# Kernel tuning notes

Hardware: AMD Instinct MI355X
Metric: run time of the kernel (lower is better)

The kernel has to match this reference:

```python
import jax, jax.numpy as jnp
import numpy as np

B, T, K, H = 256, 2048, 64, 256
NUM_PRED = 512


def setup_inputs() -> dict:
    key = jax.random.key(0)
    ks = jax.random.split(key, 13)
    s = 0.05
    G = 4 * H
    return {
        "input": jax.random.normal(ks[0], (B, T), jnp.float32),
        "conv_w": jax.random.normal(ks[1], (K,), jnp.float32) * s,
        "conv_b": jax.random.normal(ks[2], (K,), jnp.float32) * s,
        "W_ih0": jax.random.normal(ks[3], (G, K), jnp.float32) * s,
        "W_hh0": jax.random.normal(ks[4], (G, H), jnp.float32) * s,
        "b_ih0": jax.random.normal(ks[5], (G,), jnp.float32) * s,
        "b_hh0": jax.random.normal(ks[6], (G,), jnp.float32) * s,
        "W_ih1": jax.random.normal(ks[7], (G, H), jnp.float32) * s,
        "W_hh1": jax.random.normal(ks[8], (G, H), jnp.float32) * s,
        "b_ih1": jax.random.normal(ks[9], (G,), jnp.float32) * s,
        "b_hh1": jax.random.normal(ks[10], (G,), jnp.float32) * s,
        "lin_w": jax.random.normal(ks[11], (1, H), jnp.float32) * s,
        "lin_b": jax.random.normal(ks[12], (1,), jnp.float32) * s,
        "num_predictions": NUM_PRED,
    }


def _cell(x, h, c, Wi, Wh, bi, bh):
    # PyTorch LSTM cell: gate order i, f, g, o
    g = x @ Wi.T + h @ Wh.T + bi + bh
    i, f, gg, o = jnp.split(g, 4, axis=-1)
    i = jax.nn.sigmoid(i)
    f = jax.nn.sigmoid(f)
    gg = jnp.tanh(gg)
    o = jax.nn.sigmoid(o)
    c_new = f * c + i * gg
    h_new = o * jnp.tanh(c_new)
    return h_new, c_new


def reference(input, conv_w, conv_b, W_ih0, W_hh0, b_ih0, b_hh0,
              W_ih1, W_hh1, b_ih1, b_hh1, lin_w, lin_b, num_predictions):
    Bn, Tn = input.shape
    Kn = conv_w.shape[0]
    Hh = W_hh0.shape[1]

    # cnn: [B,1,T] -> Conv1d(1,K,1) -> [B,K,T] -> ReLU -> torch.reshape to (B,T,K)
    # NOTE: original uses reshape (not transpose); replicate faithfully.
    c_raw = jax.nn.relu(input[:, None, :] * conv_w[None, :, None] + conv_b[None, :, None])  # [B,K,T]
    c_out = c_raw.reshape(Bn, Tn, Kn)  # faithful reshape-as-in-source

    def step(carry, x):
        h0, c0, h1, c1 = carry
        h0, c0 = _cell(x, h0, c0, W_ih0, W_hh0, b_ih0, b_hh0)
        h1, c1 = _cell(h0, h1, c1, W_ih1, W_hh1, b_ih1, b_hh1)
        return (h0, c0, h1, c1), None

    z = jnp.zeros((Bn, Hh), input.dtype)
    carry, _ = jax.lax.scan(step, (z, z, z, z), jnp.swapaxes(c_out, 0, 1))  # scan over T
    pred0 = carry[2] @ lin_w.T + lin_b  # [B,1], output of last warmup step

    def ar_step(carry, _):
        h0, c0, h1, c1, last = carry
        x = jax.nn.relu(last[:, None] * conv_w[None, :] + conv_b[None, :])  # [B,K]
        h0, c0 = _cell(x, h0, c0, W_ih0, W_hh0, b_ih0, b_hh0)
        h1, c1 = _cell(h0, h1, c1, W_ih1, W_hh1, b_ih1, b_hh1)
        p = (h1 @ lin_w.T + lin_b)[:, 0]  # [B]
        return (h0, c0, h1, c1, p), p

    init = (*carry, pred0[:, 0])
    _, preds = jax.lax.scan(ar_step, init, None, length=num_predictions - 1)  # [P-1, B]
    return jnp.concatenate([pred0, preds.T], axis=1)  # [B, num_predictions]
```

## Files before the change

### kernel.cpp

```cpp
#include <hip/hip_runtime.h>
#include <hip/hip_bf16.h>
#include <cstdint>

#define TT 2048
#define NPRED 512
#define NSTEP (TT + NPRED)

typedef _Float16 f16;
typedef __attribute__((ext_vector_type(8))) _Float16 f16x8;
typedef __attribute__((ext_vector_type(4))) float f32x4;

#define WB0_OFF   0u
#define WB1_OFF   655360u
#define BIAS0_OFF 1703936u
#define BIAS1_OFF 1708032u
#define HX0_OFF   1712128u
#define HX1_OFF   1974272u
#define FLAG_OFF  2236416u
#define PACC_OFF  2244608u

static __device__ __forceinline__ float sigmoidf_(float x) {
    return 1.0f / (1.0f + __expf(-x));
}

static __device__ __forceinline__ uint2 ld8u(const unsigned short* p) {
    unsigned long long v = __hip_atomic_load((const unsigned long long*)p,
                                             __ATOMIC_RELAXED, __HIP_MEMORY_SCOPE_AGENT);
    uint2 r; r.x = (unsigned)v; r.y = (unsigned)(v >> 32); return r;
}
static __device__ __forceinline__ float ld1a(const float* p) {
    unsigned v = __hip_atomic_load((const unsigned*)p,
                                   __ATOMIC_RELAXED, __HIP_MEMORY_SCOPE_AGENT);
    return __uint_as_float(v);
}
static __device__ __forceinline__ void st1a(float* p, float v) {
    __hip_atomic_store((unsigned*)p, __float_as_uint(v),
                       __ATOMIC_RELAXED, __HIP_MEMORY_SCOPE_AGENT);
}
static __device__ __forceinline__ void st4a(unsigned* p, unsigned v) {
    __hip_atomic_store(p, v, __ATOMIC_RELAXED, __HIP_MEMORY_SCOPE_AGENT);
}
static __device__ __forceinline__ unsigned short f16bits(float x) {
    union { f16 h; unsigned short u; } cv;
    cv.h = (f16)x;
    return cv.u;
}

#define N0_ELEM 327680
#define N1_ELEM 524288

__global__ __launch_bounds__(256) void prep_kernel(
    const float* __restrict__ W_ih0, const float* __restrict__ W_hh0,
    const float* __restrict__ b_ih0, const float* __restrict__ b_hh0,
    const float* __restrict__ W_ih1, const float* __restrict__ W_hh1,
    const float* __restrict__ b_ih1, const float* __restrict__ b_hh1,
    f16* __restrict__ WB0, f16* __restrict__ WB1,
    float* __restrict__ bias0P, float* __restrict__ bias1P,
    unsigned int* __restrict__ flags, float* __restrict__ p_part)
{
    int idx = blockIdx.x * 256 + threadIdx.x;
    if (idx < N0_ELEM) {
        int e = idx & 7, l = (idx >> 3) & 63;
        int rest = idx >> 9;
        int fr = rest % 10, sw = rest / 10;
        int w = sw & 3, slice = sw >> 2;
        int q = l & 3, jj = (l & 15) >> 2;
        int row = q * 256 + slice * 16 + 4 * w + jj;
        int k = fr * 32 + (l >> 4) * 8 + e;
        float v = (k < 64) ? W_ih0[row * 64 + k] : W_hh0[row * 256 + (k - 64)];
        WB0[idx] = (f16)v;
    } else if (idx < N0_ELEM + N1_ELEM) {
        int i2 = idx - N0_ELEM;
        int e = i2 & 7, l = (i2 >> 3) & 63;
        int rest = i2 >> 9;
        int fr = rest & 15, sw = rest >> 4;
        int w = sw & 3, slice = sw >> 2;
        int q = l & 3, jj = (l & 15) >> 2;
        int row = q * 256 + slice * 16 + 4 * w + jj;
        int k = fr * 32 + (l >> 4) * 8 + e;
        float v = (k < 256) ? W_ih1[row * 256 + k] : W_hh1[row * 256 + (k - 256)];
        WB1[i2] = (f16)v;
    } else if (idx < N0_ELEM + N1_ELEM + 1024) {
        int r = idx - (N0_ELEM + N1_ELEM);
        int j = r >> 2, q = r & 3;
        bias0P[r] = b_ih0[q * 256 + j] + b_hh0[q * 256 + j];
    } else if (idx < N0_ELEM + N1_ELEM + 2048) {
        int r = idx - (N0_ELEM + N1_ELEM + 1024);
        int j = r >> 2, q = r & 3;
        bias1P[r] = b_ih1[q * 256 + j] + b_hh1[q * 256 + j];
    } else if (idx < N0_ELEM + N1_ELEM + 2048 + 2048) {
        flags[idx - (N0_ELEM + N1_ELEM + 2048)] = 0u;
    } else if (idx < N0_ELEM + N1_ELEM + 2048 + 2048 + 8192) {
        p_part[idx - (N0_ELEM + N1_ELEM + 2048 + 2048)] = 0.f;
    }
}

__global__ __launch_bounds__(256) void fused_kernel(
    const float* __restrict__ input,
    const float* __restrict__ conv_w, const float* __restrict__ conv_b,
    const f16* __restrict__ WB0, const f16* __restrict__ WB1,
    const float* __restrict__ bias0P, const float* __restrict__ bias1P,
    const float* __restrict__ lin_w, const float* __restrict__ lin_b,
    unsigned short* hx0, unsigned short* hx1,
    unsigned int* flags, float* p_part,
    float* __restrict__ out)
{
    const int t = threadIdx.x;
    const int lane = t & 63, w = t >> 6;
    const int g = blockIdx.x & 15, slice = blockIdx.x >> 4;

    __shared__ __align__(16) f16 Ah[18 * 65 * 8];
    __shared__ __align__(16) float gbuf0[16 * 68 + 4];
    __shared__ __align__(16) float gbuf1[16 * 68 + 4];
    __shared__ float cw_s[64], cb_s[64], lw_s[256];
    __shared__ float p_lds[16];

    f16x8 B0[10], B1[16];
    {
        const f16* p0 = WB0 + ((size_t)(slice * 4 + w) * 10 * 64 + lane) * 8;
        #pragma unroll
        for (int f = 0; f < 10; ++f) B0[f] = *(const f16x8*)(p0 + f * 512);
        const f16* p1 = WB1 + ((size_t)(slice * 4 + w) * 16 * 64 + lane) * 8;
        #pragma unroll
        for (int f = 0; f < 16; ++f) B1[f] = *(const f16x8*)(p1 + f * 512);
    }

    if (t < 64) { cw_s[t] = conv_w[t]; cb_s[t] = conv_b[t]; }
    lw_s[t] = lin_w[t];

    #pragma unroll
    for (int i = 0; i < 4; ++i) {
        int c = t + 256 * i;
        int d = ((2 + (c >> 6)) * 65 + (c & 63)) * 8;
        f16x8 z = {};
        *(f16x8*)(Ah + d) = z;
    }

    const int ub = t >> 4, uj = t & 15;
    const int jg = slice * 16 + uj;
    const float4 bs0 = *(const float4*)(bias0P + 4 * jg);
    const float4 bs1 = *(const float4*)(bias1P + 4 * jg);
    float c0 = 0.f, c1 = 0.f;
    const float linb = lin_b[0];

    const int rb = t & 15;
    const int rest = t >> 4;
    const int bg0 = g * 16;

    unsigned int* fl0 = flags + (size_t)g * 64;
    unsigned int* cnp = flags + (size_t)(16 + g) * 64;

    __syncthreads();

    #pragma unroll 1
    for (int k = 0; k < TT; ++k) {
        if (k >= 1) {
            const unsigned short* s0 = hx0 + (size_t)((k - 1) & 1) * 65536 + (size_t)(bg0 + rb) * 256;
            #pragma unroll
            for (int it = 0; it < 2; ++it) {
                int oct = rest + 16 * it;
                uint2 a = ld8u(s0 + oct * 8);
                uint2 b = ld8u(s0 + oct * 8 + 4);
                int d = ((2 + (oct >> 2)) * 65 + (rb + 16 * (oct & 3))) * 8;
                *(uint4*)(Ah + d) = make_uint4(a.x, a.y, b.x, b.y);
            }
        }
        if (k >= 2) {
            const unsigned short* s1 = hx1 + (size_t)((k - 1) & 1) * 65536 + (size_t)(bg0 + rb) * 256;
            #pragma unroll
            for (int it = 0; it < 2; ++it) {
                int oct = rest + 16 * it;
                uint2 a = ld8u(s1 + oct * 8);
                uint2 b = ld8u(s1 + oct * 8 + 4);
                int d = ((10 + (oct >> 2)) * 65 + (rb + 16 * (oct & 3))) * 8;
                *(uint4*)(Ah + d) = make_uint4(a.x, a.y, b.x, b.y);
            }
        }
        if (t < 128) {
            int rb2 = t & 15, xoct = t >> 4;
            int k0 = xoct * 8;
            const float* inprow = input + (size_t)(bg0 + rb2) * TT + ((k & 31) << 6);
            float cwv = cw_s[k >> 5], cbv = cb_s[k >> 5];
            f16x8 hv;
            #pragma unroll
            for (int e = 0; e < 8; ++e)
                hv[e] = (f16)fmaxf(inprow[k0 + e] * cwv + cbv, 0.f);
            int d = ((xoct >> 2) * 65 + (rb2 + 16 * (xoct & 3))) * 8;
            *(f16x8*)(Ah + d) = hv;
        }
        __syncthreads();

        {
            f32x4 acc = {0.f, 0.f, 0.f, 0.f};
            #pragma unroll
            for (int f = 0; f < 10; ++f) {
                f16x8 a = *(const f16x8*)(Ah + (f * 65 + lane) * 8);
                acc = __builtin_amdgcn_mfma_f32_16x16x32_f16(a, B0[f], acc, 0, 0, 0);
            }
            int rr = w * 16 + (lane & 15);
            int bb = (lane >> 4) * 4;
            #pragma unroll
            for (int qq = 0; qq < 4; ++qq) gbuf0[(bb + qq) * 68 + rr] = acc[qq];
        }
        if (k >= 1) {
            f32x4 acc = {0.f, 0.f, 0.f, 0.f};
            #pragma unroll
            for (int f = 0; f < 16; ++f) {
                f16x8 a = *(const f16x8*)(Ah + ((2 + f) * 65 + lane) * 8);
                acc = __builtin_amdgcn_mfma_f32_16x16x32_f16(a, B1[f], acc, 0, 0, 0);
            }
            int rr = w * 16 + (lane & 15);
            int bb = (lane >> 4) * 4;
            #pragma unroll
            for (int qq = 0; qq < 4; ++qq) gbuf1[(bb + qq) * 68 + rr] = acc[qq];
        }
        __syncthreads();

        {
            float4 gv = *(const float4*)(gbuf0 + ub * 68 + uj * 4);
            float gi = gv.x + bs0.x, gf = gv.y + bs0.y, gg = gv.z + bs0.z, go = gv.w + bs0.w;
            float cn = sigmoidf_(gf) * c0 + sigmoidf_(gi) * tanhf(gg);
            float hn = sigmoidf_(go) * tanhf(cn);
            c0 = cn;
            unsigned short hb = f16bits(hn);
            int oth = __shfl_xor((int)hb, 1);
            if (!(uj & 1)) {
                unsigned word = (unsigned)hb | ((unsigned)(oth & 0xffff) << 16);
                st4a((unsigned*)(hx0 + (size_t)(k & 1) * 65536 + (size_t)(bg0 + ub) * 256 + jg), word);
            }
        }
        if (k >= 1) {
            float4 gv = *(const float4*)(gbuf1 + ub * 68 + uj * 4);
            float gi = gv.x + bs1.x, gf = gv.y + bs1.y, gg = gv.z + bs1.z, go = gv.w + bs1.w;
            float cn = sigmoidf_(gf) * c1 + sigmoidf_(gi) * tanhf(gg);
            float hn = sigmoidf_(go) * tanhf(cn);
            c1 = cn;
            unsigned short hb = f16bits(hn);
            int oth = __shfl_xor((int)hb, 1);
            if (!(uj & 1)) {
                unsigned word = (unsigned)hb | ((unsigned)(oth & 0xffff) << 16);
                st4a((unsigned*)(hx1 + (size_t)(k & 1) * 65536 + (size_t)(bg0 + ub) * 256 + jg), word);
            }
        }
        __syncthreads();
        if (t == 0) {
            __hip_atomic_fetch_add(fl0, 1u, __ATOMIC_RELAXED, __HIP_MEMORY_SCOPE_AGENT);
            unsigned tgt = 16u * (unsigned)(k + 1);
            while (__hip_atomic_load(fl0, __ATOMIC_RELAXED, __HIP_MEMORY_SCOPE_AGENT) < tgt)
                __builtin_amdgcn_s_sleep(1);
        }
        __syncthreads();
    }

    #pragma unroll 1
    for (int k = TT; k < NSTEP; ++k) {
        {
            const unsigned short* s0 = hx0 + (size_t)((k - 1) & 1) * 65536 + (size_t)(bg0 + rb) * 256;
            const unsigned short* s1 = hx1 + (size_t)((k - 1) & 1) * 65536 + (size_t)(bg0 + rb) * 256;
            #pragma unroll
            for (int it = 0; it < 2; ++it) {
                int oct = rest + 16 * it;
                uint2 a0 = ld8u(s0 + oct * 8);
                uint2 b0 = ld8u(s0 + oct * 8 + 4);
                int d = ((2 + (oct >> 2)) * 65 + (rb + 16 * (oct & 3))) * 8;
                *(uint4*)(Ah + d) = make_uint4(a0.x, a0.y, b0.x, b0.y);
                uint2 a1 = ld8u(s1 + oct * 8);
                uint2 b1 = ld8u(s1 + oct * 8 + 4);
                d = ((10 + (oct >> 2)) * 65 + (rb + 16 * (oct & 3))) * 8;
                *(uint4*)(Ah + d) = make_uint4(a1.x, a1.y, b1.x, b1.y);
            }
        }
        __syncthreads();

        {
            f32x4 acc = {0.f, 0.f, 0.f, 0.f};
            #pragma unroll
            for (int f = 0; f < 16; ++f) {
                f16x8 a = *(const f16x8*)(Ah + ((2 + f) * 65 + lane) * 8);
                acc = __builtin_amdgcn_mfma_f32_16x16x32_f16(a, B1[f], acc, 0, 0, 0);
            }
            int rr = w * 16 + (lane & 15);
            int bb = (lane >> 4) * 4;
            #pragma unroll
            for (int qq = 0; qq < 4; ++qq) gbuf1[(bb + qq) * 68 + rr] = acc[qq];
        }
        __syncthreads();

        {
            float4 gv = *(const float4*)(gbuf1 + ub * 68 + uj * 4);
            float gi = gv.x + bs1.x, gf = gv.y + bs1.y, gg = gv.z + bs1.z, go = gv.w + bs1.w;
            float cn = sigmoidf_(gf) * c1 + sigmoidf_(gi) * tanhf(gg);
            float hn = sigmoidf_(go) * tanhf(cn);
            c1 = cn;
            unsigned short hb = f16bits(hn);
            int oth = __shfl_xor((int)hb, 1);
            if (!(uj & 1)) {
                unsigned word = (unsigned)hb | ((unsigned)(oth & 0xffff) << 16);
                st4a((unsigned*)(hx1 + (size_t)(k & 1) * 65536 + (size_t)(bg0 + ub) * 256 + jg), word);
            }
            float pp = hn * lw_s[jg];
            pp += __shfl_xor(pp, 1);
            pp += __shfl_xor(pp, 2);
            pp += __shfl_xor(pp, 4);
            pp += __shfl_xor(pp, 8);
            if (uj == 0)
                st1a(p_part + (size_t)(k & 1) * 4096 + (size_t)slice * 256 + (bg0 + ub), pp);
        }
        __syncthreads();
        if (t == 0) {
            __hip_atomic_fetch_add(cnp, 1u, __ATOMIC_RELAXED, __HIP_MEMORY_SCOPE_AGENT);
            unsigned tgt = 16u * (unsigned)(k - TT + 1);
            while (__hip_atomic_load(cnp, __ATOMIC_RELAXED, __HIP_MEMORY_SCOPE_AGENT) < tgt)
                __builtin_amdgcn_s_sleep(1);
        }
        __syncthreads();

        if (t < 16) {
            const float* pb = p_part + (size_t)(k & 1) * 4096;
            float ps = 0.f;
            #pragma unroll
            for (int sl = 0; sl < 16; ++sl) ps += ld1a(pb + sl * 256 + bg0 + t);
            float p = ps + linb;
            p_lds[t] = p;
            if (slice == 0) out[(size_t)(bg0 + t) * NPRED + (k - TT)] = p;
        }
        if (k == NSTEP - 1) break;
        __syncthreads();

        if (t < 128) {
            int rb2 = t & 15, xoct = t >> 4;
            int k0 = xoct * 8;
            float p = p_lds[rb2];
            f16x8 hv;
            #pragma unroll
            for (int e = 0; e < 8; ++e)
                hv[e] = (f16)fmaxf(p * cw_s[k0 + e] + cb_s[k0 + e], 0.f);
            int d = ((xoct >> 2) * 65 + (rb2 + 16 * (xoct & 3))) * 8;
            *(f16x8*)(Ah + d) = hv;
        }
        __syncthreads();

        {
            f32x4 acc = {0.f, 0.f, 0.f, 0.f};
            #pragma unroll
            for (int f = 0; f < 10; ++f) {
                f16x8 a = *(const f16x8*)(Ah + (f * 65 + lane) * 8);
                acc = __builtin_amdgcn_mfma_f32_16x16x32_f16(a, B0[f], acc, 0, 0, 0);
            }
            int rr = w * 16 + (lane & 15);
            int bb = (lane >> 4) * 4;
            #pragma unroll
            for (int qq = 0; qq < 4; ++qq) gbuf0[(bb + qq) * 68 + rr] = acc[qq];
        }
        __syncthreads();
        {
            float4 gv = *(const float4*)(gbuf0 + ub * 68 + uj * 4);
            float gi = gv.x + bs0.x, gf = gv.y + bs0.y, gg = gv.z + bs0.z, go = gv.w + bs0.w;
            float cn = sigmoidf_(gf) * c0 + sigmoidf_(gi) * tanhf(gg);
            float hn = sigmoidf_(go) * tanhf(cn);
            c0 = cn;
            unsigned short hb = f16bits(hn);
            int oth = __shfl_xor((int)hb, 1);
            if (!(uj & 1)) {
                unsigned word = (unsigned)hb | ((unsigned)(oth & 0xffff) << 16);
                st4a((unsigned*)(hx0 + (size_t)(k & 1) * 65536 + (size_t)(bg0 + ub) * 256 + jg), word);
            }
        }
        __syncthreads();
        if (t == 0) {
            __hip_atomic_fetch_add(fl0, 1u, __ATOMIC_RELAXED, __HIP_MEMORY_SCOPE_AGENT);
            unsigned tgt = 16u * (unsigned)(k + 1);
            while (__hip_atomic_load(fl0, __ATOMIC_RELAXED, __HIP_MEMORY_SCOPE_AGENT) < tgt)
                __builtin_amdgcn_s_sleep(1);
        }
        __syncthreads();
    }
}

extern "C" void kernel_launch(void* const* d_in, const int* in_sizes, int n_in,
                              void* d_out, int out_size, void* d_ws, size_t ws_size,
                              hipStream_t stream) {
    const float* input  = (const float*)d_in[0];
    const float* conv_w = (const float*)d_in[1];
    const float* conv_b = (const float*)d_in[2];
    const float* W_ih0  = (const float*)d_in[3];
    const float* W_hh0  = (const float*)d_in[4];
    const float* b_ih0  = (const float*)d_in[5];
    const float* b_hh0  = (const float*)d_in[6];
    const float* W_ih1  = (const float*)d_in[7];
    const float* W_hh1  = (const float*)d_in[8];
    const float* b_ih1  = (const float*)d_in[9];
    const float* b_hh1  = (const float*)d_in[10];
    const float* lin_w  = (const float*)d_in[11];
    const float* lin_b  = (const float*)d_in[12];
    float* out = (float*)d_out;

    uint8_t* ws = (uint8_t*)d_ws;
    f16* WB0 = (f16*)(ws + WB0_OFF);
    f16* WB1 = (f16*)(ws + WB1_OFF);
    float* bias0P = (float*)(ws + BIAS0_OFF);
    float* bias1P = (float*)(ws + BIAS1_OFF);
    unsigned short* hx0 = (unsigned short*)(ws + HX0_OFF);
    unsigned short* hx1 = (unsigned short*)(ws + HX1_OFF);
    unsigned int* flags = (unsigned int*)(ws + FLAG_OFF);
    float* p_part = (float*)(ws + PACC_OFF);

    prep_kernel<<<3376, 256, 0, stream>>>(W_ih0, W_hh0, b_ih0, b_hh0,
                                          W_ih1, W_hh1, b_ih1, b_hh1,
                                          WB0, WB1, bias0P, bias1P, flags, p_part);

    fused_kernel<<<256, 256, 0, stream>>>(input, conv_w, conv_b,
                                          WB0, WB1, bias0P, bias1P,
                                          lin_w, lin_b, hx0, hx1, flags, p_part, out);
}
```

Baseline: 9.296 ms.

## Transpose hidden-state exchange layout to feature-pair-major and compute two units per thread

The global hidden-state exchange buffers change from batch-major f16 to feature-pair-major 32-bit words. Each of 128 threads now computes two hidden units and writes a packed word directly, with no shuffle to pair halves. Each reader thread issues 4 coalesced 8-byte atomic loads per layer and scatters them into the MFMA LDS layout, instead of 4 scattered loads per row. The prediction partial sum now reduces across waves through a small LDS buffer, which adds one extra barrier per autoregressive step.

```diff
diff --git a/kernel.cpp b/kernel.cpp
--- a/kernel.cpp
+++ b/kernel.cpp
@@ -9,6 +9,7 @@
 typedef _Float16 f16;
 typedef __attribute__((ext_vector_type(8))) _Float16 f16x8;
 typedef __attribute__((ext_vector_type(4))) float f32x4;
+typedef unsigned long long u64;
 
 #define WB0_OFF   0u
 #define WB1_OFF   655360u
@@ -23,10 +24,8 @@
     return 1.0f / (1.0f + __expf(-x));
 }
 
-static __device__ __forceinline__ uint2 ld8u(const unsigned short* p) {
-    unsigned long long v = __hip_atomic_load((const unsigned long long*)p,
-                                             __ATOMIC_RELAXED, __HIP_MEMORY_SCOPE_AGENT);
-    uint2 r; r.x = (unsigned)v; r.y = (unsigned)(v >> 32); return r;
+static __device__ __forceinline__ u64 lda8w(const u64* p) {
+    return __hip_atomic_load(p, __ATOMIC_RELAXED, __HIP_MEMORY_SCOPE_AGENT);
 }
 static __device__ __forceinline__ float ld1a(const float* p) {
     unsigned v = __hip_atomic_load((const unsigned*)p,
@@ -101,7 +100,7 @@
     const f16* __restrict__ WB0, const f16* __restrict__ WB1,
     const float* __restrict__ bias0P, const float* __restrict__ bias1P,
     const float* __restrict__ lin_w, const float* __restrict__ lin_b,
-    unsigned short* hx0, unsigned short* hx1,
+    unsigned* hx0w, unsigned* hx1w,
     unsigned int* flags, float* p_part,
     float* __restrict__ out)
 {
@@ -112,8 +111,9 @@
     __shared__ __align__(16) f16 Ah[18 * 65 * 8];
     __shared__ __align__(16) float gbuf0[16 * 68 + 4];
     __shared__ __align__(16) float gbuf1[16 * 68 + 4];
-    __shared__ float cw_s[64], cb_s[64], lw_s[256];
+    __shared__ float cw_s[64], cb_s[64];
     __shared__ float p_lds[16];
+    __shared__ float p_part4[2][16];
 
     f16x8 B0[10], B1[16];
     {
@@ -126,7 +126,6 @@
     }
 
     if (t < 64) { cw_s[t] = conv_w[t]; cb_s[t] = conv_b[t]; }
-    lw_s[t] = lin_w[t];
 
     #pragma unroll
     for (int i = 0; i < 4; ++i) {
@@ -136,15 +135,21 @@
         *(f16x8*)(Ah + d) = z;
     }
 
-    const int ub = t >> 4, uj = t & 15;
-    const int jg = slice * 16 + uj;
-    const float4 bs0 = *(const float4*)(bias0P + 4 * jg);
-    const float4 bs1 = *(const float4*)(bias1P + 4 * jg);
-    float c0 = 0.f, c1 = 0.f;
+    const int jploc = t >> 4;
+    const int ucol  = t & 15;
+    const int jga   = slice * 16 + jploc * 2;
+    float4 ba0 = make_float4(0.f,0.f,0.f,0.f), bb0 = ba0, ba1 = ba0, bb1 = ba0;
+    float lwa = 0.f, lwb = 0.f;
+    if (t < 128) {
+        ba0 = *(const float4*)(bias0P + 4 * jga);
+        bb0 = *(const float4*)(bias0P + 4 * jga + 4);
+        ba1 = *(const float4*)(bias1P + 4 * jga);
+        bb1 = *(const float4*)(bias1P + 4 * jga + 4);
+        lwa = lin_w[jga];
+        lwb = lin_w[jga + 1];
+    }
+    float c0a = 0.f, c0b = 0.f, c1a = 0.f, c1b = 0.f;
     const float linb = lin_b[0];
-
-    const int rb = t & 15;
-    const int rest = t >> 4;
     const int bg0 = g * 16;
 
     unsigned int* fl0 = flags + (size_t)g * 64;
@@ -155,25 +160,31 @@
     #pragma unroll 1
     for (int k = 0; k < TT; ++k) {
         if (k >= 1) {
-            const unsigned short* s0 = hx0 + (size_t)((k - 1) & 1) * 65536 + (size_t)(bg0 + rb) * 256;
-            #pragma unroll
-            for (int it = 0; it < 2; ++it) {
-                int oct = rest + 16 * it;
-                uint2 a = ld8u(s0 + oct * 8);
-                uint2 b = ld8u(s0 + oct * 8 + 4);
-                int d = ((2 + (oct >> 2)) * 65 + (rb + 16 * (oct & 3))) * 8;
-                *(uint4*)(Ah + d) = make_uint4(a.x, a.y, b.x, b.y);
+            const unsigned* s0 = hx0w + (size_t)((k - 1) & 1) * 32768;
+            #pragma unroll
+            for (int p = 0; p < 4; ++p) {
+                int row = p * 32 + (t >> 3);
+                int cp  = t & 7;
+                u64 v = lda8w((const u64*)(s0 + row * 256 + bg0 + 2 * cp));
+                int f  = 2 + (row >> 4);
+                int la = 2 * cp + 16 * ((row & 15) >> 2);
+                int byte = (f * 65 + la) * 16 + 4 * (row & 3);
+                *(unsigned*)((char*)Ah + byte)      = (unsigned)v;
+                *(unsigned*)((char*)Ah + byte + 16) = (unsigned)(v >> 32);
             }
         }
         if (k >= 2) {
-            const unsigned short* s1 = hx1 + (size_t)((k - 1) & 1) * 65536 + (size_t)(bg0 + rb) * 256;
-            #pragma unroll
-            for (int it = 0; it < 2; ++it) {
-                int oct = rest + 16 * it;
-                uint2 a = ld8u(s1 + oct * 8);
-                uint2 b = ld8u(s1 + oct * 8 + 4);
-                int d = ((10 + (oct >> 2)) * 65 + (rb + 16 * (oct & 3))) * 8;
-                *(uint4*)(Ah + d) = make_uint4(a.x, a.y, b.x, b.y);
+            const unsigned* s1 = hx1w + (size_t)((k - 1) & 1) * 32768;
+            #pragma unroll
+            for (int p = 0; p < 4; ++p) {
+                int row = p * 32 + (t >> 3);
+                int cp  = t & 7;
+                u64 v = lda8w((const u64*)(s1 + row * 256 + bg0 + 2 * cp));
+                int f  = 10 + (row >> 4);
+                int la = 2 * cp + 16 * ((row & 15) >> 2);
+                int byte = (f * 65 + la) * 16 + 4 * (row & 3);
+                *(unsigned*)((char*)Ah + byte)      = (unsigned)v;
+                *(unsigned*)((char*)Ah + byte + 16) = (unsigned)(v >> 32);
             }
         }
         if (t < 128) {
@@ -216,30 +227,30 @@
         }
         __syncthreads();
 
-        {
-            float4 gv = *(const float4*)(gbuf0 + ub * 68 + uj * 4);
-            float gi = gv.x + bs0.x, gf = gv.y + bs0.y, gg = gv.z + bs0.z, go = gv.w + bs0.w;
-            float cn = sigmoidf_(gf) * c0 + sigmoidf_(gi) * tanhf(gg);
-            float hn = sigmoidf_(go) * tanhf(cn);
-            c0 = cn;
-            unsigned short hb = f16bits(hn);
-            int oth = __shfl_xor((int)hb, 1);
-            if (!(uj & 1)) {
-                unsigned word = (unsigned)hb | ((unsigned)(oth & 0xffff) << 16);
-                st4a((unsigned*)(hx0 + (size_t)(k & 1) * 65536 + (size_t)(bg0 + ub) * 256 + jg), word);
-            }
-        }
-        if (k >= 1) {
-            float4 gv = *(const float4*)(gbuf1 + ub * 68 + uj * 4);
-            float gi = gv.x + bs1.x, gf = gv.y + bs1.y, gg = gv.z + bs1.z, go = gv.w + bs1.w;
-            float cn = sigmoidf_(gf) * c1 + sigmoidf_(gi) * tanhf(gg);
-            float hn = sigmoidf_(go) * tanhf(cn);
-            c1 = cn;
-            unsigned short hb = f16bits(hn);
-            int oth = __shfl_xor((int)hb, 1);
-            if (!(uj & 1)) {
-                unsigned word = (unsigned)hb | ((unsigned)(oth & 0xffff) << 16);
-                st4a((unsigned*)(hx1 + (size_t)(k & 1) * 65536 + (size_t)(bg0 + ub) * 256 + jg), word);
+        if (t < 128) {
+            const float* gp = gbuf0 + ucol * 68 + jploc * 8;
+            float4 g0 = *(const float4*)(gp);
+            float4 g1 = *(const float4*)(gp + 4);
+            float cna = sigmoidf_(g0.y + ba0.y) * c0a + sigmoidf_(g0.x + ba0.x) * tanhf(g0.z + ba0.z);
+            float hna = sigmoidf_(g0.w + ba0.w) * tanhf(cna);
+            c0a = cna;
+            float cnb = sigmoidf_(g1.y + bb0.y) * c0b + sigmoidf_(g1.x + bb0.x) * tanhf(g1.z + bb0.z);
+            float hnb = sigmoidf_(g1.w + bb0.w) * tanhf(cnb);
+            c0b = cnb;
+            unsigned word = (unsigned)f16bits(hna) | ((unsigned)f16bits(hnb) << 16);
+            st4a(hx0w + (size_t)(k & 1) * 32768 + (size_t)(slice * 8 + jploc) * 256 + (bg0 + ucol), word);
+            if (k >= 1) {
+                const float* hp = gbuf1 + ucol * 68 + jploc * 8;
+                float4 h0v = *(const float4*)(hp);
+                float4 h1v = *(const float4*)(hp + 4);
+                float cka = sigmoidf_(h0v.y + ba1.y) * c1a + sigmoidf_(h0v.x + ba1.x) * tanhf(h0v.z + ba1.z);
+                float hka = sigmoidf_(h0v.w + ba1.w) * tanhf(cka);
+                c1a = cka;
+                float ckb = sigmoidf_(h1v.y + bb1.y) * c1b + sigmoidf_(h1v.x + bb1.x) * tanhf(h1v.z + bb1.z);
+                float hkb = sigmoidf_(h1v.w + bb1.w) * tanhf(ckb);
+                c1b = ckb;
+                unsigned wrd = (unsigned)f16bits(hka) | ((unsigned)f16bits(hkb) << 16);
+                st4a(hx1w + (size_t)(k & 1) * 32768 + (size_t)(slice * 8 + jploc) * 256 + (bg0 + ucol), wrd);
             }
         }
         __syncthreads();
@@ -255,19 +266,21 @@
     #pragma unroll 1
     for (int k = TT; k < NSTEP; ++k) {
         {
-            const unsigned short* s0 = hx0 + (size_t)((k - 1) & 1) * 65536 + (size_t)(bg0 + rb) * 256;
-            const unsigned short* s1 = hx1 + (size_t)((k - 1) & 1) * 65536 + (size_t)(bg0 + rb) * 256;
-            #pragma unroll
-            for (int it = 0; it < 2; ++it) {
-                int oct = rest + 16 * it;
-                uint2 a0 = ld8u(s0 + oct * 8);
-                uint2 b0 = ld8u(s0 + oct * 8 + 4);
-                int d = ((2 + (oct >> 2)) * 65 + (rb + 16 * (oct & 3))) * 8;
-                *(uint4*)(Ah + d) = make_uint4(a0.x, a0.y, b0.x, b0.y);
-                uint2 a1 = ld8u(s1 + oct * 8);
-                uint2 b1 = ld8u(s1 + oct * 8 + 4);
-                d = ((10 + (oct >> 2)) * 65 + (rb + 16 * (oct & 3))) * 8;
-                *(uint4*)(Ah + d) = make_uint4(a1.x, a1.y, b1.x, b1.y);
+            const unsigned* s0 = hx0w + (size_t)((k - 1) & 1) * 32768;
+            const unsigned* s1 = hx1w + (size_t)((k - 1) & 1) * 32768;
+            #pragma unroll
+            for (int p = 0; p < 4; ++p) {
+                int row = p * 32 + (t >> 3);
+                int cp  = t & 7;
+                u64 v0 = lda8w((const u64*)(s0 + row * 256 + bg0 + 2 * cp));
+                int la = 2 * cp + 16 * ((row & 15) >> 2);
+                int byte0 = ((2 + (row >> 4)) * 65 + la) * 16 + 4 * (row & 3);
+                *(unsigned*)((char*)Ah + byte0)      = (unsigned)v0;
+                *(unsigned*)((char*)Ah + byte0 + 16) = (unsigned)(v0 >> 32);
+                u64 v1 = lda8w((const u64*)(s1 + row * 256 + bg0 + 2 * cp));
+                int byte1 = ((10 + (row >> 4)) * 65 + la) * 16 + 4 * (row & 3);
+                *(unsigned*)((char*)Ah + byte1)      = (unsigned)v1;
+                *(unsigned*)((char*)Ah + byte1 + 16) = (unsigned)(v1 >> 32);
             }
         }
         __syncthreads();
@@ -286,25 +299,27 @@
         }
         __syncthreads();
 
-        {
-            float4 gv = *(const float4*)(gbuf1 + ub * 68 + uj * 4);
-            float gi = gv.x + bs1.x, gf = gv.y + bs1.y, gg = gv.z + bs1.z, go = gv.w + bs1.w;
-            float cn = sigmoidf_(gf) * c1 + sigmoidf_(gi) * tanhf(gg);
-            float hn = sigmoidf_(go) * tanhf(cn);
-            c1 = cn;
-            unsigned short hb = f16bits(hn);
-            int oth = __shfl_xor((int)hb, 1);
-            if (!(uj & 1)) {
-                unsigned word = (unsigned)hb | ((unsigned)(oth & 0xffff) << 16);
-                st4a((unsigned*)(hx1 + (size_t)(k & 1) * 65536 + (size_t)(bg0 + ub) * 256 + jg), word);
-            }
-            float pp = hn * lw_s[jg];
-            pp += __shfl_xor(pp, 1);
-            pp += __shfl_xor(pp, 2);
-            pp += __shfl_xor(pp, 4);
-            pp += __shfl_xor(pp, 8);
-            if (uj == 0)
-                st1a(p_part + (size_t)(k & 1) * 4096 + (size_t)slice * 256 + (bg0 + ub), pp);
+        if (t < 128) {
+            const float* hp = gbuf1 + ucol * 68 + jploc * 8;
+            float4 h0v = *(const float4*)(hp);
+            float4 h1v = *(const float4*)(hp + 4);
+            float cka = sigmoidf_(h0v.y + ba1.y) * c1a + sigmoidf_(h0v.x + ba1.x) * tanhf(h0v.z + ba1.z);
+            float hka = sigmoidf_(h0v.w + ba1.w) * tanhf(cka);
+            c1a = cka;
+            float ckb = sigmoidf_(h1v.y + bb1.y) * c1b + sigmoidf_(h1v.x + bb1.x) * tanhf(h1v.z + bb1.z);
+            float hkb = sigmoidf_(h1v.w + bb1.w) * tanhf(ckb);
+            c1b = ckb;
+            unsigned wrd = (unsigned)f16bits(hka) | ((unsigned)f16bits(hkb) << 16);
+            st4a(hx1w + (size_t)(k & 1) * 32768 + (size_t)(slice * 8 + jploc) * 256 + (bg0 + ucol), wrd);
+            float pp = hka * lwa + hkb * lwb;
+            pp += __shfl_xor(pp, 16);
+            pp += __shfl_xor(pp, 32);
+            if ((lane & 48) == 0) p_part4[w][ucol] = pp;
+        }
+        __syncthreads();
+        if (t < 16) {
+            float s4 = p_part4[0][t] + p_part4[1][t];
+            st1a(p_part + (size_t)(k & 1) * 4096 + (size_t)slice * 256 + (bg0 + t), s4);
         }
         __syncthreads();
         if (t == 0) {
@@ -353,18 +368,18 @@
             for (int qq = 0; qq < 4; ++qq) gbuf0[(bb + qq) * 68 + rr] = acc[qq];
         }
         __syncthreads();
-        {
-            float4 gv = *(const float4*)(gbuf0 + ub * 68 + uj * 4);
-            float gi = gv.x + bs0.x, gf = gv.y + bs0.y, gg = gv.z + bs0.z, go = gv.w + bs0.w;
-            float cn = sigmoidf_(gf) * c0 + sigmoidf_(gi) * tanhf(gg);
-            float hn = sigmoidf_(go) * tanhf(cn);
-            c0 = cn;
-            unsigned short hb = f16bits(hn);
-            int oth = __shfl_xor((int)hb, 1);
-            if (!(uj & 1)) {
-                unsigned word = (unsigned)hb | ((unsigned)(oth & 0xffff) << 16);
-                st4a((unsigned*)(hx0 + (size_t)(k & 1) * 65536 + (size_t)(bg0 + ub) * 256 + jg), word);
-            }
+        if (t < 128) {
+            const float* gp = gbuf0 + ucol * 68 + jploc * 8;
+            float4 g0 = *(const float4*)(gp);
+            float4 g1 = *(const float4*)(gp + 4);
+            float cna = sigmoidf_(g0.y + ba0.y) * c0a + sigmoidf_(g0.x + ba0.x) * tanhf(g0.z + ba0.z);
+            float hna = sigmoidf_(g0.w + ba0.w) * tanhf(cna);
+            c0a = cna;
+            float cnb = sigmoidf_(g1.y + bb0.y) * c0b + sigmoidf_(g1.x + bb0.x) * tanhf(g1.z + bb0.z);
+            float hnb = sigmoidf_(g1.w + bb0.w) * tanhf(cnb);
+            c0b = cnb;
+            unsigned word = (unsigned)f16bits(hna) | ((unsigned)f16bits(hnb) << 16);
+            st4a(hx0w + (size_t)(k & 1) * 32768 + (size_t)(slice * 8 + jploc) * 256 + (bg0 + ucol), word);
         }
         __syncthreads();
         if (t == 0) {
@@ -400,8 +415,8 @@
     f16* WB1 = (f16*)(ws + WB1_OFF);
     float* bias0P = (float*)(ws + BIAS0_OFF);
     float* bias1P = (float*)(ws + BIAS1_OFF);
-    unsigned short* hx0 = (unsigned short*)(ws + HX0_OFF);
-    unsigned short* hx1 = (unsigned short*)(ws + HX1_OFF);
+    unsigned* hx0w = (unsigned*)(ws + HX0_OFF);
+    unsigned* hx1w = (unsigned*)(ws + HX1_OFF);
     unsigned int* flags = (unsigned int*)(ws + FLAG_OFF);
     float* p_part = (float*)(ws + PACC_OFF);
 
@@ -411,5 +426,5 @@
 
     fused_kernel<<<256, 256, 0, stream>>>(input, conv_w, conv_b,
                                           WB0, WB1, bias0P, bias1P,
-                                          lin_w, lin_b, hx0, hx1, flags, p_part, out);
-}
+                                          lin_w, lin_b, hx0w, hx1w, flags, p_part, out);
+}
```

Measured after the change: 11.44 ms. +23.0%, slower.
